# Optimization experiments

Hardware: AMD Instinct MI355X
Metric: run time of the kernel (lower is better)

The kernel has to match this reference:

```python
import jax, jax.numpy as jnp
import numpy as np

NUM_HEADS = 16
HEAD_DIM = 128
ROPE_BASE = 10000.0


def rotate_half(x):
    x1, x2 = jnp.split(x, 2, axis=-1)
    return jnp.concatenate((-x2, x1), axis=-1)


def rope_cos_sin(seq_len, dim, dtype):
    inv_freq = 1.0 / (ROPE_BASE ** (jnp.arange(0, dim, 2, dtype=jnp.float32) / dim))
    t = jnp.arange(seq_len, dtype=jnp.float32)
    freqs = jnp.einsum('i,j->ij', t, inv_freq)          # [S, dim/2]
    emb = jnp.concatenate((freqs, freqs), axis=-1)       # [S, dim]
    return emb.astype(dtype)  # caller applies cos/sin


def setup_inputs() -> dict:
    key = jax.random.key(0)
    k0, k1, k2, k3, k4 = jax.random.split(key, 5)
    B, S, H = 2, 2048, 2048
    hd = H // NUM_HEADS
    scale = 0.02
    return {
        'hidden_states': jax.random.normal(k0, (B, S, H), dtype=jnp.float32),
        'Wq': jax.random.normal(k1, (H, H), dtype=jnp.float32) * scale,
        'Wk': jax.random.normal(k2, (hd, H), dtype=jnp.float32) * scale,
        'Wv': jax.random.normal(k3, (hd, H), dtype=jnp.float32) * scale,
        'Wo': jax.random.normal(k4, (H, H), dtype=jnp.float32) * scale,
    }


def reference(hidden_states, Wq, Wk, Wv, Wo):
    B, S, H = hidden_states.shape
    nH, hd = NUM_HEADS, HEAD_DIM

    # projections (torch Linear: x @ W.T)
    q = jnp.einsum('bsh,oh->bso', hidden_states, Wq).reshape(B, S, nH, hd)
    q = q.transpose(0, 2, 1, 3)                          # [B, nH, S, hd]
    k = jnp.einsum('bsh,dh->bsd', hidden_states, Wk)      # [B, S, hd] single KV head
    v = jnp.einsum('bsh,dh->bsd', hidden_states, Wv)      # [B, S, hd]

    # rotary embedding
    emb = rope_cos_sin(S, hd, hidden_states.dtype)        # [S, hd]
    cos, sin = jnp.cos(emb), jnp.sin(emb)
    q = q * cos[None, None] + rotate_half(q) * sin[None, None]
    k = k * cos[None] + rotate_half(k) * sin[None]

    # attention: Q heads against shared K/V head
    scores = jnp.einsum('bhqd,bkd->bhqk', q, k) / jnp.sqrt(jnp.asarray(hd, hidden_states.dtype))
    attn = jax.nn.softmax(scores, axis=-1)               # dropout is identity in eval
    out = jnp.einsum('bhqk,bkd->bhqd', attn, v)           # [B, nH, S, hd]
    out = out.transpose(0, 2, 1, 3).reshape(B, S, H)
    attn_output = jnp.einsum('bsh,oh->bso', out, Wo)

    # cache tensors returned by the torch module: k, v with head dim of 1
    return attn_output, k[:, None], v[:, None]
```

## Files before the change

### kernel.cpp

```cpp
#include <hip/hip_runtime.h>
#include <hip/hip_bf16.h>

typedef __hip_bfloat16 bf16;

#define NH   16
#define HD   128
#define SEQ  2048
#define BB   2
#define HID  2048

#define ROPE_C 0.14391156856f

using frag   = __attribute__((ext_vector_type(8))) short;
using f32x4  = __attribute__((ext_vector_type(4))) float;
using f32x16 = __attribute__((ext_vector_type(16))) float;


__device__ __forceinline__ void cvt8_store(const float4 f0, const float4 f1, bf16* dst) {
    union { frag v; bf16 h[8]; } p;
    p.h[0] = __float2bfloat16(f0.x); p.h[1] = __float2bfloat16(f0.y);
    p.h[2] = __float2bfloat16(f0.z); p.h[3] = __float2bfloat16(f0.w);
    p.h[4] = __float2bfloat16(f1.x); p.h[5] = __float2bfloat16(f1.y);
    p.h[6] = __float2bfloat16(f1.z); p.h[7] = __float2bfloat16(f1.w);
    *reinterpret_cast<frag*>(dst) = p.v;
}

__device__ __forceinline__ unsigned pk2(float a, float b) {
    union { bf16 h[2]; unsigned u; } p;
    p.h[0] = __float2bfloat16(a);
    p.h[1] = __float2bfloat16(b);
    return p.u;
}

__global__ __launch_bounds__(512) void gemm_qkv(const float* __restrict__ A,
                                                const float* __restrict__ Wq,
                                                const float* __restrict__ Wk,
                                                const float* __restrict__ Wv,
                                                bf16* __restrict__ qout,
                                                float* __restrict__ Ck,
                                                float* __restrict__ Cv,
                                                bf16* __restrict__ kb,
                                                bf16* __restrict__ vt) {
    __shared__ bf16 Asl[4096];
    __shared__ bf16 Bsl[4096];
    const int tid  = threadIdx.x;
    const int wave = tid >> 6;
    const int lane = tid & 63;
    const int quad = lane >> 4;
    const int l15  = lane & 15;
    const int row0 = blockIdx.y * 128;
    const int bx   = blockIdx.x;
    const bool isq  = bx < 16;
    const bool is_v = (bx == 17);
    const float* W  = isq ? Wq : (is_v ? Wv : Wk);
    const int col0  = isq ? bx * 128 : 0;

    const int sr = tid >> 2;
    const int sc = (tid & 3) * 8;

    f32x4 acc[8];
#pragma unroll
    for (int j = 0; j < 8; ++j) acc[j] = (f32x4){0.f,0.f,0.f,0.f};

    for (int k0 = 0; k0 < HID; k0 += 32) {
        __syncthreads();
        {
            const float4* a0 = reinterpret_cast<const float4*>(A + (size_t)(row0 + sr) * HID + k0 + sc);
            const float4* b0 = reinterpret_cast<const float4*>(W + (size_t)(col0 + sr) * HID + k0 + sc);
            cvt8_store(a0[0], a0[1], &Asl[tid * 8]);
            cvt8_store(b0[0], b0[1], &Bsl[tid * 8]);
        }
        __syncthreads();
        frag af, bfr[8];
        af = *reinterpret_cast<const frag*>(&Asl[(((wave*16 + l15)*4) + quad) * 8]);
#pragma unroll
        for (int j = 0; j < 8; ++j)
            bfr[j] = *reinterpret_cast<const frag*>(&Bsl[(((j*16 + l15)*4) + quad) * 8]);
#pragma unroll
        for (int j = 0; j < 8; ++j)
            acc[j] = __builtin_amdgcn_mfma_f32_16x16x32_bf16(af, bfr[j], acc[j], 0, 0, 0);
    }

    if (isq) {
#pragma unroll
        for (int r = 0; r < 4; ++r) {
            const int row = row0 + wave*16 + quad*4 + r;
            const int s = row & (SEQ - 1);
            bf16* crow = qout + (size_t)row * HID + col0;
#pragma unroll
            for (int j = 0; j < 4; ++j) {
                const int d = 16*j + l15;
                const float invf = expf(-(float)d * ROPE_C);
                float sn, cs;
                sincosf((float)s * invf, &sn, &cs);
                const float x1 = acc[j][r], x2 = acc[j+4][r];
                crow[d]      = __float2bfloat16(x1*cs - x2*sn);
                crow[d + 64] = __float2bfloat16(x2*cs + x1*sn);
            }
        }
    } else if (is_v) {
#pragma unroll
        for (int r = 0; r < 4; ++r) {
            const int row = row0 + wave*16 + quad*4 + r;
            const int s = row & (SEQ - 1);
            const int b = row >> 11;
            float* crow = Cv + (size_t)row * HD;
#pragma unroll
            for (int j = 0; j < 8; ++j) {
                const int d = 16*j + l15;
                const float val = acc[j][r];
                crow[d] = val;
                vt[((size_t)b * HD + d) * SEQ + s] = __float2bfloat16(val);
            }
        }
    } else {
#pragma unroll
        for (int r = 0; r < 4; ++r) {
            const int row = row0 + wave*16 + quad*4 + r;
            const int s = row & (SEQ - 1);
            float* crow = Ck + (size_t)row * HD;
#pragma unroll
            for (int j = 0; j < 4; ++j) {
                const int d = 16*j + l15;
                const float invf = expf(-(float)d * ROPE_C);
                float sn, cs;
                sincosf((float)s * invf, &sn, &cs);
                const float y1 = acc[j][r]*cs - acc[j+4][r]*sn;
                const float y2 = acc[j+4][r]*cs + acc[j][r]*sn;
                crow[d]      = y1;
                crow[d + 64] = y2;
                kb[(size_t)row * HD + d]      = __float2bfloat16(y1);
                kb[(size_t)row * HD + d + 64] = __float2bfloat16(y2);
            }
        }
    }
}

__global__ __launch_bounds__(256) void attn_mfma(const bf16* __restrict__ qbuf,
                                                 const bf16* __restrict__ kb,
                                                 const bf16* __restrict__ vt,
                                                 bf16* __restrict__ attn_out) {
    __shared__ char lds[32768];

    const int tid  = threadIdx.x;
    const int wave = tid >> 6;
    const int lane = tid & 63;
    const int l31  = lane & 31;
    const int h    = lane >> 5;
    const int qg   = wave & 1;
    const int kg   = wave >> 1;
    const int q0   = blockIdx.x * 64;
    const int hh   = blockIdx.y;
    const int b    = blockIdx.z;

    const bf16* kbb = kb + (size_t)b * SEQ * HD;
    const bf16* vtb = vt + (size_t)b * HD * SEQ;

    frag qfr[8];
    {
        const bf16* qrow = qbuf + ((size_t)(b * SEQ + q0 + qg * 32 + l31)) * HID + hh * HD;
#pragma unroll
        for (int c = 0; c < 8; ++c)
            qfr[c] = *reinterpret_cast<const frag*>(qrow + c * 16 + h * 8);
    }

    const int sl   = tid & 127;
    const int kg_s = tid >> 7;

    int klof[4];
#pragma unroll
    for (int i = 0; i < 4; ++i) {
        const int n   = sl + i * 128;
        const int key = n >> 4, d = (n >> 1) & 7, hs = n & 1;
        const int L   = d * 64 + key * 2 + hs;
        klof[i] = (kg_s * 8192 + L * 16) ^ (((((key >> 2) ^ d) & 7)) << 4);
    }
    int vlof[8], vgof[8];
#pragma unroll
    for (int i = 0; i < 8; ++i) {
        const int g   = sl + i * 128;
        const int dim = g >> 3, ks = (g >> 2) & 1, m = (g >> 1) & 1, hs = g & 1;
        const int dt  = dim >> 5;
        const int C   = (dt * 2 + ks) * 64 + (dim & 31) * 2 + hs;
        const int B   = 16384 + kg_s * 8192 + C * 16 + m * 8;
        const int xv  = (((dim & 31) >> 2) ^ (dt * 2 + ks)) & 7;
        vlof[i] = B ^ (xv << 4);
        vgof[i] = dim * SEQ + kg_s * 32 + (g & 7) * 4;
    }

    const int rpos = (l31 * 2 + h) * 16;
    const int rsw  = rpos ^ ((((rpos >> 7) & 7)) << 4);

    f32x16 oacc[4];
#pragma unroll
    for (int dt = 0; dt < 4; ++dt)
#pragma unroll
        for (int r = 0; r < 16; ++r) oacc[dt][r] = 0.f;
    float mrow = -1e30f;
    float lrow = 0.f;
    const float scale = 0.088388347648318433f;

    for (int it = 0; it < SEQ / 64; ++it) {
        __syncthreads();
        {
            const bf16* kp = kbb + (size_t)it * 64 * HD + kg_s * 4096;
            const bf16* vp = vtb + it * 64;
            uint4 krg[4];
            uint2 vrg[8];
#pragma unroll
            for (int i = 0; i < 4; ++i)
                krg[i] = *reinterpret_cast<const uint4*>(kp + (sl + i * 128) * 8);
#pragma unroll
            for (int i = 0; i < 8; ++i)
                vrg[i] = *reinterpret_cast<const uint2*>(vp + vgof[i]);
#pragma unroll
            for (int i = 0; i < 4; ++i)
                *reinterpret_cast<uint4*>(lds + klof[i]) = krg[i];
#pragma unroll
            for (int i = 0; i < 8; ++i)
                *reinterpret_cast<uint2*>(lds + vlof[i]) = vrg[i];
        }
        __syncthreads();

        f32x16 sacc;
#pragma unroll
        for (int r = 0; r < 16; ++r) sacc[r] = 0.f;
#pragma unroll
        for (int c = 0; c < 8; ++c) {
            const frag kf = *reinterpret_cast<const frag*>(
                lds + kg * 8192 + c * 1024 + (rsw ^ (c << 4)));
            sacc = __builtin_amdgcn_mfma_f32_32x32x16_bf16(kf, qfr[c], sacc, 0, 0, 0);
        }

        float mx = -1e30f;
#pragma unroll
        for (int r = 0; r < 16; ++r) mx = fmaxf(mx, sacc[r]);
        mx = fmaxf(mx, __shfl_xor(mx, 32));
        const bool skip = (bool)__all(mx - mrow <= 90.0f);
        const float mn = skip ? mrow : fmaxf(mrow, mx);
        const float al = skip ? 1.f : __expf((mrow - mn) * scale);
        float p[16];
        float ps = 0.f;
#pragma unroll
        for (int r = 0; r < 16; ++r) {
            p[r] = __expf((sacc[r] - mn) * scale);
            ps += p[r];
        }
        ps += __shfl_xor(ps, 32);
        lrow = lrow * al + ps;
        mrow = mn;

        frag pb[2];
#pragma unroll
        for (int ks = 0; ks < 2; ++ks) {
            union { unsigned u[4]; frag f; } pf;
#pragma unroll
            for (int w = 0; w < 4; ++w)
                pf.u[w] = pk2(p[8 * ks + 2 * w], p[8 * ks + 2 * w + 1]);
            pb[ks] = pf.f;
        }

        if (!skip)
#pragma unroll
            for (int dt = 0; dt < 4; ++dt)
#pragma unroll
                for (int r = 0; r < 16; ++r) oacc[dt][r] *= al;

#pragma unroll
        for (int dt = 0; dt < 4; ++dt)
#pragma unroll
            for (int ks = 0; ks < 2; ++ks) {
                const int cb = dt * 2 + ks;
                const frag vf = *reinterpret_cast<const frag*>(
                    lds + 16384 + kg * 8192 + cb * 1024 + (rsw ^ (cb << 4)));
                oacc[dt] = __builtin_amdgcn_mfma_f32_32x32x16_bf16(vf, pb[ks], oacc[dt], 0, 0, 0);
            }
    }

    __syncthreads();
    float* fl = reinterpret_cast<float*>(lds);
    if (h == 0) {
        fl[(qg * 2 + kg) * 32 + l31]       = mrow;
        fl[128 + (qg * 2 + kg) * 32 + l31] = lrow;
    }
    __syncthreads();
    const float m0 = fl[qg * 64 + l31],       m1 = fl[qg * 64 + 32 + l31];
    const float l0 = fl[128 + qg * 64 + l31], l1 = fl[128 + qg * 64 + 32 + l31];
    const float ms = fmaxf(m0, m1);
    const float c0 = __expf((m0 - ms) * scale);
    const float c1 = __expf((m1 - ms) * scale);
    const float inv = 1.f / (c0 * l0 + c1 * l1);
    const float cs = kg ? c1 : c0;
#pragma unroll
    for (int dt = 0; dt < 4; ++dt)
#pragma unroll
        for (int r = 0; r < 16; ++r) oacc[dt][r] *= cs;

    float* ob = reinterpret_cast<float*>(lds + 1024);
#pragma unroll
    for (int dt = 0; dt < 4; ++dt) {
        __syncthreads();
        if (kg == 1) {
            float* dst = ob + (qg * 64 + lane) * 17;
#pragma unroll
            for (int r = 0; r < 16; ++r) dst[r] = oacc[dt][r];
        }
        __syncthreads();
        if (kg == 0) {
            const float* sp = ob + (qg * 64 + lane) * 17;
            const int s = q0 + qg * 32 + l31;
            bf16* orow = attn_out + ((size_t)(b * SEQ + s)) * HID + hh * HD;
#pragma unroll
            for (int t = 0; t < 4; ++t) {
                const float v0 = (oacc[dt][t*4+0] + sp[t*4+0]) * inv;
                const float v1 = (oacc[dt][t*4+1] + sp[t*4+1]) * inv;
                const float v2 = (oacc[dt][t*4+2] + sp[t*4+2]) * inv;
                const float v3 = (oacc[dt][t*4+3] + sp[t*4+3]) * inv;
                uint2 val;
                val.x = pk2(v0, v1);
                val.y = pk2(v2, v3);
                *reinterpret_cast<uint2*>(orow + dt * 32 + t * 8 + h * 4) = val;
            }
        }
    }
}

__global__ __launch_bounds__(512) void gemm_o_mfma(const bf16* __restrict__ A,
                                                   const float* __restrict__ W,
                                                   float* __restrict__ C) {
    __shared__ bf16 Asl[4096];
    __shared__ bf16 Bsl[4096];
    const int tid  = threadIdx.x;
    const int wave = tid >> 6;
    const int lane = tid & 63;
    const int quad = lane >> 4;
    const int l15  = lane & 15;
    const int row0 = blockIdx.y * 128;
    const int col0 = blockIdx.x * 128;

    const int sr = tid >> 2;
    const int sc = (tid & 3) * 8;

    f32x4 acc[8];
#pragma unroll
    for (int j = 0; j < 8; ++j) acc[j] = (f32x4){0.f,0.f,0.f,0.f};

    for (int k0 = 0; k0 < HID; k0 += 32) {
        __syncthreads();
        {
            *reinterpret_cast<uint4*>(&Asl[tid * 8]) =
                *reinterpret_cast<const uint4*>(A + (size_t)(row0 + sr) * HID + k0 + sc);
            const float4* b0 = reinterpret_cast<const float4*>(W + (size_t)(col0 + sr) * HID + k0 + sc);
            cvt8_store(b0[0], b0[1], &Bsl[tid * 8]);
        }
        __syncthreads();
        frag af, bfr[8];
        af = *reinterpret_cast<const frag*>(&Asl[(((wave*16 + l15)*4) + quad) * 8]);
#pragma unroll
        for (int j = 0; j < 8; ++j)
            bfr[j] = *reinterpret_cast<const frag*>(&Bsl[(((j*16 + l15)*4) + quad) * 8]);
#pragma unroll
        for (int j = 0; j < 8; ++j)
            acc[j] = __builtin_amdgcn_mfma_f32_16x16x32_bf16(af, bfr[j], acc[j], 0, 0, 0);
    }

#pragma unroll
    for (int r = 0; r < 4; ++r) {
        const int row = row0 + wave*16 + quad*4 + r;
        float* crow = C + (size_t)row * HID + col0;
#pragma unroll
        for (int j = 0; j < 8; ++j)
            crow[16*j + l15] = acc[j][r];
    }
}

extern "C" void kernel_launch(void* const* d_in, const int* in_sizes, int n_in,
                              void* d_out, int out_size, void* d_ws, size_t ws_size,
                              hipStream_t stream) {
    const float* hs = (const float*)d_in[0];
    const float* Wq = (const float*)d_in[1];
    const float* Wk = (const float*)d_in[2];
    const float* Wv = (const float*)d_in[3];
    const float* Wo = (const float*)d_in[4];

    float* out      = (float*)d_out;
    float* out_attn = out;
    float* out_k    = out + 8388608;
    float* out_v    = out + 8388608 + 524288;

    bf16* qbuf = (bf16*)d_out;
    bf16* kb   = (bf16*)((char*)d_out + 16777216);
    bf16* vt   = (bf16*)((char*)d_out + 17825792);
    bf16* attn_out = (bf16*)d_ws;

    gemm_qkv  <<<dim3(18, (BB*SEQ)/128), dim3(512), 0, stream>>>(hs, Wq, Wk, Wv,
                                                                 qbuf, out_k, out_v, kb, vt);
    attn_mfma <<<dim3(SEQ/64, NH, BB),   dim3(256), 0, stream>>>(qbuf, kb, vt, attn_out);
    gemm_o_mfma<<<dim3(HID/128, (BB*SEQ)/128), dim3(512), 0, stream>>>(attn_out, Wo, out_attn);
}
```

Before: 392.0 us.

## Pre-convert QKV inputs to bf16 and load GEMM tiles directly into LDS

A new kernel converts hidden_states and the Q/K/V weights from fp32 to bf16 in one pass, writing into spare output and workspace regions. The QKV GEMM then streams bf16 tiles straight into shared memory with global_load_lds. This replaces the per-tile fp32 loads and in-register conversions, and halves the bytes each repeated tile read moves. The O-projection GEMM uses the same direct-to-LDS load for its bf16 activation tile. The cost is an extra launch plus a full read and write pass over the inputs, and the code relies on aliasing output and workspace buffers that later kernels overwrite.

```diff
diff --git a/kernel.cpp b/kernel.cpp
--- a/kernel.cpp
+++ b/kernel.cpp
@@ -32,10 +32,37 @@
     return p.u;
 }
 
-__global__ __launch_bounds__(512) void gemm_qkv(const float* __restrict__ A,
+__device__ __forceinline__ void gld_lds16(const bf16* g, bf16* l) {
+    __builtin_amdgcn_global_load_lds(
+        (const __attribute__((address_space(1))) void*)g,
+        (__attribute__((address_space(3))) void*)l, 16, 0, 0);
+}
+
+__global__ __launch_bounds__(256) void cvt_bf16(const float* __restrict__ hs,
                                                 const float* __restrict__ Wq,
                                                 const float* __restrict__ Wk,
                                                 const float* __restrict__ Wv,
+                                                bf16* __restrict__ hsb,
+                                                bf16* __restrict__ wqb,
+                                                bf16* __restrict__ wkb,
+                                                bf16* __restrict__ wvb) {
+    const int blk = blockIdx.x;
+    const float* src;
+    bf16* dst;
+    if (blk < 4096)      { src = hs + (size_t)blk * 2048;          dst = hsb + (size_t)blk * 2048; }
+    else if (blk < 6144) { src = Wq + (size_t)(blk - 4096) * 2048; dst = wqb + (size_t)(blk - 4096) * 2048; }
+    else if (blk < 6272) { src = Wk + (size_t)(blk - 6144) * 2048; dst = wkb + (size_t)(blk - 6144) * 2048; }
+    else                 { src = Wv + (size_t)(blk - 6272) * 2048; dst = wvb + (size_t)(blk - 6272) * 2048; }
+    const int t = threadIdx.x * 8;
+    const float4 f0 = *reinterpret_cast<const float4*>(src + t);
+    const float4 f1 = *reinterpret_cast<const float4*>(src + t + 4);
+    cvt8_store(f0, f1, dst + t);
+}
+
+__global__ __launch_bounds__(512) void gemm_qkv(const bf16* __restrict__ A,
+                                                const bf16* __restrict__ Wqb,
+                                                const bf16* __restrict__ Wkb,
+                                                const bf16* __restrict__ Wvb,
                                                 bf16* __restrict__ qout,
                                                 float* __restrict__ Ck,
                                                 float* __restrict__ Cv,
@@ -52,24 +79,25 @@
     const int bx   = blockIdx.x;
     const bool isq  = bx < 16;
     const bool is_v = (bx == 17);
-    const float* W  = isq ? Wq : (is_v ? Wv : Wk);
+    const bf16* W   = isq ? Wqb : (is_v ? Wvb : Wkb);
     const int col0  = isq ? bx * 128 : 0;
 
     const int sr = tid >> 2;
     const int sc = (tid & 3) * 8;
 
+    const bf16* ag = A + (size_t)(row0 + sr) * HID + sc;
+    const bf16* bg = W + (size_t)(col0 + sr) * HID + sc;
+    bf16* al = &Asl[tid * 8];
+    bf16* bl = &Bsl[tid * 8];
+
     f32x4 acc[8];
 #pragma unroll
     for (int j = 0; j < 8; ++j) acc[j] = (f32x4){0.f,0.f,0.f,0.f};
 
     for (int k0 = 0; k0 < HID; k0 += 32) {
         __syncthreads();
-        {
-            const float4* a0 = reinterpret_cast<const float4*>(A + (size_t)(row0 + sr) * HID + k0 + sc);
-            const float4* b0 = reinterpret_cast<const float4*>(W + (size_t)(col0 + sr) * HID + k0 + sc);
-            cvt8_store(a0[0], a0[1], &Asl[tid * 8]);
-            cvt8_store(b0[0], b0[1], &Bsl[tid * 8]);
-        }
+        gld_lds16(ag + k0, al);
+        gld_lds16(bg + k0, bl);
         __syncthreads();
         frag af, bfr[8];
         af = *reinterpret_cast<const frag*>(&Asl[(((wave*16 + l15)*4) + quad) * 8]);
@@ -341,15 +369,17 @@
     const int sr = tid >> 2;
     const int sc = (tid & 3) * 8;
 
+    const bf16* ag = A + (size_t)(row0 + sr) * HID + sc;
+    bf16* al = &Asl[tid * 8];
+
     f32x4 acc[8];
 #pragma unroll
     for (int j = 0; j < 8; ++j) acc[j] = (f32x4){0.f,0.f,0.f,0.f};
 
     for (int k0 = 0; k0 < HID; k0 += 32) {
         __syncthreads();
+        gld_lds16(ag + k0, al);
         {
-            *reinterpret_cast<uint4*>(&Asl[tid * 8]) =
-                *reinterpret_cast<const uint4*>(A + (size_t)(row0 + sr) * HID + k0 + sc);
             const float4* b0 = reinterpret_cast<const float4*>(W + (size_t)(col0 + sr) * HID + k0 + sc);
             cvt8_store(b0[0], b0[1], &Bsl[tid * 8]);
         }
@@ -391,10 +421,15 @@
     bf16* qbuf = (bf16*)d_out;
     bf16* kb   = (bf16*)((char*)d_out + 16777216);
     bf16* vt   = (bf16*)((char*)d_out + 17825792);
+    bf16* wqb  = (bf16*)((char*)d_out + 18874368);
+    bf16* wkb  = (bf16*)((char*)d_out + 27262976);
+    bf16* wvb  = (bf16*)((char*)d_out + 27787264);
+    bf16* hsb      = (bf16*)d_ws;
     bf16* attn_out = (bf16*)d_ws;
 
-    gemm_qkv  <<<dim3(18, (BB*SEQ)/128), dim3(512), 0, stream>>>(hs, Wq, Wk, Wv,
-                                                                 qbuf, out_k, out_v, kb, vt);
-    attn_mfma <<<dim3(SEQ/64, NH, BB),   dim3(256), 0, stream>>>(qbuf, kb, vt, attn_out);
+    cvt_bf16  <<<dim3(6400),                  dim3(256), 0, stream>>>(hs, Wq, Wk, Wv, hsb, wqb, wkb, wvb);
+    gemm_qkv  <<<dim3(18, (BB*SEQ)/128),      dim3(512), 0, stream>>>(hsb, wqb, wkb, wvb,
+                                                                      qbuf, out_k, out_v, kb, vt);
+    attn_mfma <<<dim3(SEQ/64, NH, BB),        dim3(256), 0, stream>>>(qbuf, kb, vt, attn_out);
     gemm_o_mfma<<<dim3(HID/128, (BB*SEQ)/128), dim3(512), 0, stream>>>(attn_out, Wo, out_attn);
 }
```

Measured after the change: 377.7 us. -3.6%, faster.
